# Kernel tuning notes

Measured on AMD Instinct MI355X. Metric: run time of the kernel, lower is better.

Reference implementation:

```python
import jax, jax.numpy as jnp
import numpy as np
import math

N_EMBD = 1024
N_HEAD = 16
BLOCK_SIZE = 2048
B, T = 4, 2048

def setup_inputs() -> dict:
    key = jax.random.key(0)
    ks = jax.random.split(key, 5)
    s = 0.02
    x = jax.random.normal(ks[0], (B, T, N_EMBD), dtype=jnp.float32)
    W_attn = jax.random.normal(ks[1], (N_EMBD, 3 * N_EMBD), dtype=jnp.float32) * s
    b_attn = jnp.zeros((3 * N_EMBD,), dtype=jnp.float32)
    W_proj = jax.random.normal(ks[2], (N_EMBD, N_EMBD), dtype=jnp.float32) * s
    b_proj = jnp.zeros((N_EMBD,), dtype=jnp.float32)
    return {"x": x, "W_attn": W_attn, "b_attn": b_attn, "W_proj": W_proj, "b_proj": b_proj}

def reference(x, W_attn, b_attn, W_proj, b_proj):
    b, t, c = x.shape
    hd = c // N_HEAD  # head dim
    qkv = x @ W_attn + b_attn                      # [B,T,3C]
    q, k, v = jnp.split(qkv, 3, axis=-1)
    # [B,T,C] -> [B,H,T,hd]
    q = q.reshape(b, t, N_HEAD, hd).transpose(0, 2, 1, 3)
    k = k.reshape(b, t, N_HEAD, hd).transpose(0, 2, 1, 3)
    v = v.reshape(b, t, N_HEAD, hd).transpose(0, 2, 1, 3)
    att = jnp.einsum('bhqd,bhkd->bhqk', q, k) * (1.0 / math.sqrt(hd))
    causal = jnp.tril(jnp.ones((t, t), dtype=bool))
    att = jnp.where(causal[None, None], att, -jnp.inf)
    att = jax.nn.softmax(att, axis=-1)
    y = jnp.einsum('bhqk,bhkd->bhqd', att, v)      # [B,H,T,hd]
    y = y.transpose(0, 2, 1, 3).reshape(b, t, c)
    return y @ W_proj + b_proj
```

## Files before the change

### kernel.cpp

```cpp
#include <hip/hip_runtime.h>

typedef unsigned short u16;
typedef __bf16 bf16x8 __attribute__((ext_vector_type(8)));
typedef float    f32x4 __attribute__((ext_vector_type(4)));
typedef unsigned short u16x8 __attribute__((ext_vector_type(8)));

__device__ __forceinline__ float bf2f(u16 v){ return __uint_as_float(((unsigned int)v) << 16); }
__device__ __forceinline__ u16 f2bf(float f){
    unsigned int u = __float_as_uint(f);
    u += 0x7fffu + ((u >> 16) & 1u);
    return (u16)(u >> 16);
}
__device__ __forceinline__ u16 f2bf_t(float f){ return (u16)(__float_as_uint(f) >> 16); }
__device__ __forceinline__ unsigned pack_trunc(float hi, float lo){
    return __builtin_amdgcn_perm(__float_as_uint(hi), __float_as_uint(lo), 0x07060302);
}
__device__ __forceinline__ float exp2_fast(float x){
    float r; asm("v_exp_f32 %0, %1" : "=v"(r) : "v"(x)); return r;
}

__device__ __forceinline__ void glds16(const u16* gp, u16* lp){
    __builtin_amdgcn_global_load_lds((unsigned int __attribute__((address_space(1)))*)gp,
                                     (unsigned int __attribute__((address_space(3)))*)lp,
                                     16, 0, 0);
}

__device__ __forceinline__ int probe_f32(const u16* __restrict__ xp){
    u16 lo = xp[2 * (threadIdx.x & 63)];
    int e = (lo >> 7) & 0xff;
    bool bad = !(e == 0 || (e > 96 && e < 160));
    return __popcll(__ballot(bad)) > 16;
}

__global__ __launch_bounds__(256) void conv_x(const void* __restrict__ src, u16* __restrict__ dst,
                                              const u16* __restrict__ xprobe){
    const int isf32 = probe_f32(xprobe);
    size_t i = ((size_t)blockIdx.x * 256 + threadIdx.x) * 8;
    if (isf32){
        const float* p = (const float*)src + i;
        float4 a = *(const float4*)p, b = *(const float4*)(p + 4);
        u16x8 o = { f2bf(a.x), f2bf(a.y), f2bf(a.z), f2bf(a.w),
                    f2bf(b.x), f2bf(b.y), f2bf(b.z), f2bf(b.w) };
        *(u16x8*)(dst + i) = o;
    } else {
        *(u16x8*)(dst + i) = *(const u16x8*)((const u16*)src + i);
    }
}

__global__ __launch_bounds__(256) void transposeW(const void* __restrict__ in, u16* __restrict__ out,
                                                  int R, int C, const u16* __restrict__ xprobe){
    __shared__ u16 t[64][65];
    const int isf32 = probe_f32(xprobe);
    const int c0 = blockIdx.x * 64, r0 = blockIdx.y * 64;
    const int tx = threadIdx.x & 15, ty = threadIdx.x >> 4;
#pragma unroll
    for (int i = 0; i < 4; i++){
        int r = ty + i * 16;
        u16 a, b, c, d;
        if (isf32){
            float4 v = *(const float4*)((const float*)in + (size_t)(r0 + r) * C + c0 + tx * 4);
            a = f2bf(v.x); b = f2bf(v.y); c = f2bf(v.z); d = f2bf(v.w);
        } else {
            ushort4 v = *(const ushort4*)((const u16*)in + (size_t)(r0 + r) * C + c0 + tx * 4);
            a = v.x; b = v.y; c = v.z; d = v.w;
        }
        t[r][tx*4+0] = a; t[r][tx*4+1] = b; t[r][tx*4+2] = c; t[r][tx*4+3] = d;
    }
    __syncthreads();
#pragma unroll
    for (int i = 0; i < 4; i++){
        int oc = ty + i * 16;
        ushort4 v;
        v.x = t[tx*4+0][oc]; v.y = t[tx*4+1][oc]; v.z = t[tx*4+2][oc]; v.w = t[tx*4+3][oc];
        *(ushort4*)(out + (size_t)(c0 + oc) * R + r0 + tx * 4) = v;
    }
}

#define CTS 136
template<int MODE>
__global__ __launch_bounds__(256) void gemm128(
    const u16* __restrict__ A, const u16* __restrict__ Bt, const void* __restrict__ bias,
    void* __restrict__ C, u16* __restrict__ Cq, u16* __restrict__ Ck, u16* __restrict__ Cv,
    const u16* __restrict__ xprobe, int M, int N, int K)
{
    __shared__ u16 Asm[128 * 32];
    __shared__ u16 Bsm[128 * 32];
    __shared__ u16 Ct[128 * CTS];
    const int isf32 = probe_f32(xprobe);
    const int tid = threadIdx.x;
    const int wave = tid >> 6, lane = tid & 63;
    const int quad = lane >> 4, ml = lane & 15;
    const int m_blk = blockIdx.y * 128;
    const int n_blk = blockIdx.x * 128;
    const int wm = (wave >> 1) * 64, wn = (wave & 1) * 64;
    const int rsub = lane >> 2;
    const int kc   = lane & 3;

    f32x4 acc[4][4];
#pragma unroll
    for (int a = 0; a < 4; a++)
#pragma unroll
        for (int b = 0; b < 4; b++)
            acc[a][b] = (f32x4){0.f, 0.f, 0.f, 0.f};

    for (int k0 = 0; k0 < K; k0 += 32){
        __syncthreads();
#pragma unroll
        for (int i = 0; i < 2; i++){
            int row = (wave * 2 + i) * 16 + rsub;
            glds16(A  + (size_t)(m_blk + row) * K + k0 + kc * 8, Asm + (wave * 2 + i) * 512);
            glds16(Bt + (size_t)(n_blk + row) * K + k0 + kc * 8, Bsm + (wave * 2 + i) * 512);
        }
        __syncthreads();
        bf16x8 af[4], bfr[4];
#pragma unroll
        for (int mt = 0; mt < 4; mt++) af[mt]  = *(const bf16x8*)&Asm[(wm + mt * 16 + ml) * 32 + quad * 8];
#pragma unroll
        for (int nt = 0; nt < 4; nt++) bfr[nt] = *(const bf16x8*)&Bsm[(wn + nt * 16 + ml) * 32 + quad * 8];
#pragma unroll
        for (int mt = 0; mt < 4; mt++)
#pragma unroll
            for (int nt = 0; nt < 4; nt++)
                acc[mt][nt] = __builtin_amdgcn_mfma_f32_16x16x32_bf16(af[mt], bfr[nt], acc[mt][nt], 0, 0, 0);
    }

    const float QSC = 0.18033688f;
    if (MODE == 0){
        const int which = n_blk >> 10;
        const int hbase = (n_blk >> 6) & 15;
        if (which < 2){
            const float sc = (which == 0) ? QSC : 1.0f;
#pragma unroll
            for (int nt = 0; nt < 4; nt++){
                int col = wn + nt * 16 + ml;
                float bv = isf32 ? ((const float*)bias)[n_blk + col] : bf2f(((const u16*)bias)[n_blk + col]);
#pragma unroll
                for (int mt = 0; mt < 4; mt++){
                    int row0 = wm + mt * 16 + quad * 4;
#pragma unroll
                    for (int r = 0; r < 4; r++)
                        Ct[(row0 + r) * CTS + col] = f2bf_t((acc[mt][nt][r] + bv) * sc);
                }
            }
            __syncthreads();
            u16* dst0 = (which == 0) ? Cq : Ck;
            const int b = m_blk >> 11, t0 = m_blk & 2047;
#pragma unroll
            for (int i = 0; i < 8; i++){
                int u = i * 256 + tid;
                int row = u >> 4, c8 = u & 15;
                int h = hbase + (c8 >> 3), d8 = (c8 & 7) * 8;
                u16x8 v = *(const u16x8*)&Ct[row * CTS + c8 * 8];
                *(u16x8*)&dst0[(((size_t)(b * 16 + h)) * 2048 + (t0 + row)) * 64 + d8] = v;
            }
        } else {
#pragma unroll
            for (int nt = 0; nt < 4; nt++){
                int col = wn + nt * 16 + ml;
                float bv = isf32 ? ((const float*)bias)[n_blk + col] : bf2f(((const u16*)bias)[n_blk + col]);
#pragma unroll
                for (int mt = 0; mt < 4; mt++){
                    int row0 = wm + mt * 16 + quad * 4;
                    uint2 pk;
                    pk.x = pack_trunc(acc[mt][nt][1] + bv, acc[mt][nt][0] + bv);
                    pk.y = pack_trunc(acc[mt][nt][3] + bv, acc[mt][nt][2] + bv);
                    *(uint2*)&Ct[col * CTS + row0] = pk;
                }
            }
            __syncthreads();
            const int b = m_blk >> 11, t0 = m_blk & 2047;
#pragma unroll
            for (int i = 0; i < 8; i++){
                int u = i * 256 + tid;
                int col = u >> 4, c8 = u & 15;
                int h = hbase + (col >> 6), d = col & 63;
                u16x8 v = *(const u16x8*)&Ct[col * CTS + c8 * 8];
                *(u16x8*)&Cv[(((size_t)(b * 16 + h)) * 64 + d) * 2048 + t0 + c8 * 8] = v;
            }
        }
    } else {
#pragma unroll
        for (int nt = 0; nt < 4; nt++){
            int col = n_blk + wn + nt * 16 + ml;
            float bv = isf32 ? ((const float*)bias)[col] : bf2f(((const u16*)bias)[col]);
#pragma unroll
            for (int mt = 0; mt < 4; mt++){
                float o0 = acc[mt][nt][0] + bv, o1 = acc[mt][nt][1] + bv;
                float o2 = acc[mt][nt][2] + bv, o3 = acc[mt][nt][3] + bv;
                int row0 = m_blk + wm + mt * 16 + quad * 4;
                if (isf32){
                    float* p = (float*)C + (size_t)row0 * N + col;
                    p[0] = o0; p[N] = o1; p[2*N] = o2; p[3*N] = o3;
                } else {
                    u16* p = (u16*)C + (size_t)row0 * N + col;
                    p[0] = f2bf(o0); p[N] = f2bf(o1); p[2*N] = f2bf(o2); p[3*N] = f2bf(o3);
                }
            }
        }
    }
}

#define PS 136
__global__ __launch_bounds__(256) void attn_kernel(
    const u16* __restrict__ Q, const u16* __restrict__ K, const u16* __restrict__ Vt,
    u16* __restrict__ Y)
{
    __shared__ u16 Ksm[128 * 64];
    __shared__ u16 Vsm[64 * 128];
    __shared__ u16 Psm[4][32 * PS];

    const int tid = threadIdx.x, wave = tid >> 6, lane = tid & 63;
    const int quad = lane >> 4, ml = lane & 15;
    const int flat = blockIdx.x;
    const int qb = 15 - (flat >> 6);
    const int rest = flat & 63;
    const int bh = ((rest & 7) << 3) | (rest >> 3);
    const int q0 = qb * 128;
    const size_t base = (size_t)bh * (2048 * 64);
    const float NEG = -1.0e30f;

    bf16x8 qf[2][2];
#pragma unroll
    for (int mt = 0; mt < 2; mt++)
#pragma unroll
        for (int ks = 0; ks < 2; ks++)
            qf[mt][ks] = *(const bf16x8*)(Q + base + (size_t)(q0 + mt * 64 + wave * 16 + ml) * 64 + ks * 32 + quad * 8);

    f32x4 acc[2][4];
#pragma unroll
    for (int mt = 0; mt < 2; mt++)
#pragma unroll
        for (int nt = 0; nt < 4; nt++) acc[mt][nt] = (f32x4){0.f, 0.f, 0.f, 0.f};
    float l[2][4];
#pragma unroll
    for (int mt = 0; mt < 2; mt++)
#pragma unroll
        for (int r = 0; r < 4; r++) l[mt][r] = 0.f;

    const int ntj = qb + 1;
    for (int j = 0; j < ntj; j++){
        const int j0 = j * 128;
        __syncthreads();
#pragma unroll
        for (int i = 0; i < 4; i++){
            int ub = i * 256 + wave * 64;
            int u = ub + lane;
            int row = u >> 3, cg = (lane & 7) ^ (row & 7);
            glds16(K + base + (size_t)(j0 + row) * 64 + cg * 8, Ksm + ub * 8);
            int d = u >> 4, vg = (lane & 15) ^ (d & 15);
            glds16(Vt + base + (size_t)d * 2048 + j0 + vg * 8, Vsm + ub * 8);
        }
        __syncthreads();
        const bool lastj = (j == ntj - 1);

#pragma unroll
        for (int nt = 0; nt < 8; nt++){
            bf16x8 bk0 = *(const bf16x8*)&Ksm[(nt * 16 + ml) * 64 + ((quad)     ^ (ml & 7)) * 8];
            bf16x8 bk1 = *(const bf16x8*)&Ksm[(nt * 16 + ml) * 64 + ((4 + quad) ^ (ml & 7)) * 8];
            f32x4 z = {0.f, 0.f, 0.f, 0.f};
            f32x4 s0 = __builtin_amdgcn_mfma_f32_16x16x32_bf16(qf[0][0], bk0, z, 0, 0, 0);
            s0 = __builtin_amdgcn_mfma_f32_16x16x32_bf16(qf[0][1], bk1, s0, 0, 0, 0);
            f32x4 s1 = __builtin_amdgcn_mfma_f32_16x16x32_bf16(qf[1][0], bk0, z, 0, 0, 0);
            s1 = __builtin_amdgcn_mfma_f32_16x16x32_bf16(qf[1][1], bk1, s1, 0, 0, 0);
            if (lastj){
                int cl = nt * 16 + ml;
                int r0 = wave * 16 + quad * 4;
#pragma unroll
                for (int r = 0; r < 4; r++){
                    if (cl > r0 + r)      s0[r] = NEG;
                    if (cl > 64 + r0 + r) s1[r] = NEG;
                }
            }
#pragma unroll
            for (int r = 0; r < 4; r++){
                float p0 = exp2_fast(s0[r]); l[0][r] += p0;
                Psm[wave][(quad * 4 + r) * PS + nt * 16 + ml] = f2bf_t(p0);
                float p1 = exp2_fast(s1[r]); l[1][r] += p1;
                Psm[wave][(16 + quad * 4 + r) * PS + nt * 16 + ml] = f2bf_t(p1);
            }
        }
#pragma unroll
        for (int ks = 0; ks < 4; ks++){
            bf16x8 pf0 = *(const bf16x8*)&Psm[wave][ml * PS + ks * 32 + quad * 8];
            bf16x8 pf1 = *(const bf16x8*)&Psm[wave][(16 + ml) * PS + ks * 32 + quad * 8];
#pragma unroll
            for (int nt = 0; nt < 4; nt++){
                bf16x8 vf = *(const bf16x8*)&Vsm[(nt * 16 + ml) * 128 + (((ks * 4 + quad) ^ ml) & 15) * 8];
                acc[0][nt] = __builtin_amdgcn_mfma_f32_16x16x32_bf16(pf0, vf, acc[0][nt], 0, 0, 0);
                acc[1][nt] = __builtin_amdgcn_mfma_f32_16x16x32_bf16(pf1, vf, acc[1][nt], 0, 0, 0);
            }
        }
    }
    const int b = bh >> 4, h = bh & 15;
#pragma unroll
    for (int mt = 0; mt < 2; mt++){
        f32x4 inv;
#pragma unroll
        for (int r = 0; r < 4; r++){
            float t = l[mt][r];
            t += __shfl_xor(t, 1, 64);
            t += __shfl_xor(t, 2, 64);
            t += __shfl_xor(t, 4, 64);
            t += __shfl_xor(t, 8, 64);
            inv[r] = 1.0f / t;
        }
#pragma unroll
        for (int nt = 0; nt < 4; nt++)
#pragma unroll
            for (int r = 0; r < 4; r++){
                size_t row = (size_t)b * 2048 + q0 + mt * 64 + wave * 16 + quad * 4 + r;
                Y[row * 1024 + h * 64 + nt * 16 + ml] = f2bf(acc[mt][nt][r] * inv[r]);
            }
    }
}

extern "C" void kernel_launch(void* const* d_in, const int* in_sizes, int n_in,
                              void* d_out, int out_size, void* d_ws, size_t ws_size,
                              hipStream_t stream) {
    const void* x      = d_in[0];
    const void* W_attn = d_in[1];
    const void* b_attn = d_in[2];
    const void* W_proj = d_in[3];
    const void* b_proj = d_in[4];
    const u16* xprobe = (const u16*)x;

    u16* ws = (u16*)d_ws;
    u16* Qw = ws;
    u16* Kw = ws + 8u * 1024 * 1024;
    u16* Vw = ws + 16u * 1024 * 1024;
    u16* R  = ws + 24u * 1024 * 1024;
    u16* Wt_attn = R;
    u16* Yw      = R;
    u16* Wt_proj = Qw;
    u16* xb = (u16*)d_out;

    conv_x<<<4096, 256, 0, stream>>>(x, xb, xprobe);
    transposeW<<<dim3(48, 16), 256, 0, stream>>>(W_attn, Wt_attn, 1024, 3072, xprobe);
    gemm128<0><<<dim3(24, 64), 256, 0, stream>>>(
        xb, Wt_attn, b_attn, nullptr, Qw, Kw, Vw, xprobe, 8192, 3072, 1024);
    attn_kernel<<<1024, 256, 0, stream>>>(Qw, Kw, Vw, Yw);
    transposeW<<<dim3(16, 16), 256, 0, stream>>>(W_proj, Wt_proj, 1024, 1024, xprobe);
    gemm128<1><<<dim3(8, 64), 256, 0, stream>>>(
        Yw, Wt_proj, b_proj, d_out, nullptr, nullptr, nullptr, xprobe, 8192, 1024, 1024);
}
```

Measured before the change: 263.6 us.

## Rewrite GEMM as 256x256 tiles with 4-stage async LDS pipeline

Replaces the 128x128 single-buffered GEMM with a 256x256-tile, 512-thread kernel. It uses a four-stage global_load_lds ring with explicit vmcnt waits and barriers, swizzled LDS layout to reduce bank conflicts, s_setprio around MFMA bursts, and XCD-aware block remapping. The goal is to hide global load latency and raise arithmetic intensity per tile. The trade-offs are 128KB of LDS and a larger accumulator register footprint, which limit occupancy. Grid counts also drop to 384 and 128 blocks, which may underfill the device for the projection GEMM.

Measured after the change: 266.6 us. No clear change (+1.1%).

```diff
diff --git a/kernel.cpp b/kernel.cpp
--- a/kernel.cpp
+++ b/kernel.cpp
@@ -76,118 +76,174 @@
     }
 }
 
-#define CTS 136
+#define BAR()    asm volatile("s_barrier" ::: "memory")
+#define WAITV(n) asm volatile("s_waitcnt vmcnt(" #n ")" ::: "memory")
+
 template<int MODE>
-__global__ __launch_bounds__(256) void gemm128(
+__global__ __launch_bounds__(512, 2) void gemm256(
     const u16* __restrict__ A, const u16* __restrict__ Bt, const void* __restrict__ bias,
     void* __restrict__ C, u16* __restrict__ Cq, u16* __restrict__ Ck, u16* __restrict__ Cv,
     const u16* __restrict__ xprobe, int M, int N, int K)
 {
-    __shared__ u16 Asm[128 * 32];
-    __shared__ u16 Bsm[128 * 32];
-    __shared__ u16 Ct[128 * CTS];
+    __shared__ u16 lds[65536];
     const int isf32 = probe_f32(xprobe);
     const int tid = threadIdx.x;
     const int wave = tid >> 6, lane = tid & 63;
     const int quad = lane >> 4, ml = lane & 15;
-    const int m_blk = blockIdx.y * 128;
-    const int n_blk = blockIdx.x * 128;
-    const int wm = (wave >> 1) * 64, wn = (wave & 1) * 64;
-    const int rsub = lane >> 2;
-    const int kc   = lane & 3;
-
-    f32x4 acc[4][4];
-#pragma unroll
-    for (int a = 0; a < 4; a++)
+    const int wm = wave >> 2, wn = wave & 3;
+
+    const int nbx = gridDim.x;
+    int flat = blockIdx.y * nbx + blockIdx.x;
+    const int cpx = (nbx * gridDim.y) >> 3;
+    flat = (flat & 7) * cpx + (flat >> 3);
+    const int m_blk = (flat / nbx) * 256;
+    const int n_blk = (flat % nbx) * 256;
+
+    const int rowb = tid >> 2;
+    const int swz  = (tid & 3) ^ ((tid >> 3) & 3);
+    const u16* a0 = A  + (size_t)(m_blk + rowb) * K + swz * 8;
+    const u16* a1 = a0 + (size_t)128 * K;
+    const u16* b0 = Bt + (size_t)(n_blk + rowb) * K + swz * 8;
+    const u16* b1 = b0 + (size_t)128 * K;
+    u16* ldA = lds + wave * 512;
+    u16* ldB = lds + 8192 + wave * 512;
+
+    const int fsw  = (quad ^ ((ml >> 1) & 3)) * 8;
+    const int aoff = (wm * 128 + ml) * 32 + fsw;
+    const int boff = (wn * 64  + ml) * 32 + fsw;
+
+    f32x4 acc[8][4];
+#pragma unroll
+    for (int a = 0; a < 8; a++)
 #pragma unroll
         for (int b = 0; b < 4; b++)
             acc[a][b] = (f32x4){0.f, 0.f, 0.f, 0.f};
 
-    for (int k0 = 0; k0 < K; k0 += 32){
-        __syncthreads();
-#pragma unroll
-        for (int i = 0; i < 2; i++){
-            int row = (wave * 2 + i) * 16 + rsub;
-            glds16(A  + (size_t)(m_blk + row) * K + k0 + kc * 8, Asm + (wave * 2 + i) * 512);
-            glds16(Bt + (size_t)(n_blk + row) * K + k0 + kc * 8, Bsm + (wave * 2 + i) * 512);
-        }
-        __syncthreads();
-        bf16x8 af[4], bfr[4];
-#pragma unroll
-        for (int mt = 0; mt < 4; mt++) af[mt]  = *(const bf16x8*)&Asm[(wm + mt * 16 + ml) * 32 + quad * 8];
-#pragma unroll
-        for (int nt = 0; nt < 4; nt++) bfr[nt] = *(const bf16x8*)&Bsm[(wn + nt * 16 + ml) * 32 + quad * 8];
-#pragma unroll
-        for (int mt = 0; mt < 4; mt++)
+    const int T = K >> 5;
+
+#define STAGE_A(t) { const int s_ = ((t) & 3) * 16384; const size_t ko_ = (size_t)(t) * 32; \
+    glds16(a0 + ko_, ldA + s_); glds16(a1 + ko_, ldA + s_ + 4096); }
+#define STAGE_B(t) { const int s_ = ((t) & 3) * 16384; const size_t ko_ = (size_t)(t) * 32; \
+    glds16(b0 + ko_, ldB + s_); glds16(b1 + ko_, ldB + s_ + 4096); }
+
+    STAGE_A(0); STAGE_B(0); STAGE_A(1); STAGE_B(1); STAGE_A(2); STAGE_B(2);
+    WAITV(8);
+    BAR();
+
+    for (int t = 0; t < T; ++t){
+        const u16* Ls = lds + (t & 3) * 16384;
+        bf16x8 af[4], bf[4];
+        if (t + 3 < T) STAGE_A(t + 3);
+#pragma unroll
+        for (int nt = 0; nt < 4; nt++) bf[nt] = *(const bf16x8*)&Ls[8192 + boff + nt * 512];
+#pragma unroll
+        for (int i = 0; i < 4; i++)    af[i] = *(const bf16x8*)&Ls[aoff + i * 512];
+        __builtin_amdgcn_s_setprio(1);
+#pragma unroll
+        for (int i = 0; i < 4; i++)
 #pragma unroll
             for (int nt = 0; nt < 4; nt++)
-                acc[mt][nt] = __builtin_amdgcn_mfma_f32_16x16x32_bf16(af[mt], bfr[nt], acc[mt][nt], 0, 0, 0);
-    }
+                acc[i][nt] = __builtin_amdgcn_mfma_f32_16x16x32_bf16(af[i], bf[nt], acc[i][nt], 0, 0, 0);
+        __builtin_amdgcn_s_setprio(0);
+        BAR();
+        if (t + 3 < T) STAGE_B(t + 3);
+#pragma unroll
+        for (int i = 0; i < 4; i++)    af[i] = *(const bf16x8*)&Ls[aoff + (4 + i) * 512];
+        __builtin_amdgcn_s_setprio(1);
+#pragma unroll
+        for (int i = 0; i < 4; i++)
+#pragma unroll
+            for (int nt = 0; nt < 4; nt++)
+                acc[4 + i][nt] = __builtin_amdgcn_mfma_f32_16x16x32_bf16(af[i], bf[nt], acc[4 + i][nt], 0, 0, 0);
+        __builtin_amdgcn_s_setprio(0);
+        if (t < T - 3)       { WAITV(8); }
+        else if (t == T - 3) { WAITV(4); }
+        else if (t == T - 2) { WAITV(0); }
+        BAR();
+    }
+#undef STAGE_A
+#undef STAGE_B
 
     const float QSC = 0.18033688f;
     if (MODE == 0){
+        __syncthreads();
         const int which = n_blk >> 10;
         const int hbase = (n_blk >> 6) & 15;
+        const int b = m_blk >> 11, t0 = m_blk & 2047;
         if (which < 2){
             const float sc = (which == 0) ? QSC : 1.0f;
-#pragma unroll
-            for (int nt = 0; nt < 4; nt++){
-                int col = wn + nt * 16 + ml;
-                float bv = isf32 ? ((const float*)bias)[n_blk + col] : bf2f(((const u16*)bias)[n_blk + col]);
-#pragma unroll
-                for (int mt = 0; mt < 4; mt++){
-                    int row0 = wm + mt * 16 + quad * 4;
-#pragma unroll
-                    for (int r = 0; r < 4; r++)
-                        Ct[(row0 + r) * CTS + col] = f2bf_t((acc[mt][nt][r] + bv) * sc);
-                }
-            }
-            __syncthreads();
             u16* dst0 = (which == 0) ? Cq : Ck;
-            const int b = m_blk >> 11, t0 = m_blk & 2047;
-#pragma unroll
-            for (int i = 0; i < 8; i++){
-                int u = i * 256 + tid;
-                int row = u >> 4, c8 = u & 15;
-                int h = hbase + (c8 >> 3), d8 = (c8 & 7) * 8;
-                u16x8 v = *(const u16x8*)&Ct[row * CTS + c8 * 8];
-                *(u16x8*)&dst0[(((size_t)(b * 16 + h)) * 2048 + (t0 + row)) * 64 + d8] = v;
+            u16* Ct = lds;
+#pragma unroll
+            for (int hn = 0; hn < 2; hn++){
+                if ((wn >> 1) == hn){
+#pragma unroll
+                    for (int nt = 0; nt < 4; nt++){
+                        int col = (wn & 1) * 64 + nt * 16 + ml;
+                        int gc  = n_blk + hn * 128 + col;
+                        float bv = isf32 ? ((const float*)bias)[gc] : bf2f(((const u16*)bias)[gc]);
+#pragma unroll
+                        for (int mt = 0; mt < 8; mt++){
+                            int row0 = wm * 128 + mt * 16 + quad * 4;
+#pragma unroll
+                            for (int r = 0; r < 4; r++)
+                                Ct[(row0 + r) * 136 + col] = f2bf_t((acc[mt][nt][r] + bv) * sc);
+                        }
+                    }
+                }
+                __syncthreads();
+#pragma unroll
+                for (int i = 0; i < 8; i++){
+                    int u = i * 512 + tid;
+                    int row = u >> 4, c8 = u & 15;
+                    int h = hbase + hn * 2 + (c8 >> 3), d8 = (c8 & 7) * 8;
+                    u16x8 v = *(const u16x8*)&Ct[row * 136 + c8 * 8];
+                    *(u16x8*)&dst0[(((size_t)(b * 16 + h)) * 2048 + (t0 + row)) * 64 + d8] = v;
+                }
+                __syncthreads();
             }
         } else {
-#pragma unroll
-            for (int nt = 0; nt < 4; nt++){
-                int col = wn + nt * 16 + ml;
-                float bv = isf32 ? ((const float*)bias)[n_blk + col] : bf2f(((const u16*)bias)[n_blk + col]);
-#pragma unroll
-                for (int mt = 0; mt < 4; mt++){
-                    int row0 = wm + mt * 16 + quad * 4;
-                    uint2 pk;
-                    pk.x = pack_trunc(acc[mt][nt][1] + bv, acc[mt][nt][0] + bv);
-                    pk.y = pack_trunc(acc[mt][nt][3] + bv, acc[mt][nt][2] + bv);
-                    *(uint2*)&Ct[col * CTS + row0] = pk;
-                }
-            }
-            __syncthreads();
-            const int b = m_blk >> 11, t0 = m_blk & 2047;
-#pragma unroll
-            for (int i = 0; i < 8; i++){
-                int u = i * 256 + tid;
-                int col = u >> 4, c8 = u & 15;
-                int h = hbase + (col >> 6), d = col & 63;
-                u16x8 v = *(const u16x8*)&Ct[col * CTS + c8 * 8];
-                *(u16x8*)&Cv[(((size_t)(b * 16 + h)) * 64 + d) * 2048 + t0 + c8 * 8] = v;
+            u16* Ct = lds;
+#pragma unroll
+            for (int hn = 0; hn < 2; hn++){
+                if ((wn >> 1) == hn){
+#pragma unroll
+                    for (int nt = 0; nt < 4; nt++){
+                        int col = (wn & 1) * 64 + nt * 16 + ml;
+                        int gc  = n_blk + hn * 128 + col;
+                        float bv = isf32 ? ((const float*)bias)[gc] : bf2f(((const u16*)bias)[gc]);
+#pragma unroll
+                        for (int mt = 0; mt < 8; mt++){
+                            int row0 = wm * 128 + mt * 16 + quad * 4;
+                            uint2 pk;
+                            pk.x = pack_trunc(acc[mt][nt][1] + bv, acc[mt][nt][0] + bv);
+                            pk.y = pack_trunc(acc[mt][nt][3] + bv, acc[mt][nt][2] + bv);
+                            *(uint2*)&Ct[col * 264 + row0] = pk;
+                        }
+                    }
+                }
+                __syncthreads();
+#pragma unroll
+                for (int i = 0; i < 8; i++){
+                    int u = i * 512 + tid;
+                    int col = u >> 5, c8 = u & 31;
+                    int h = hbase + hn * 2 + (col >> 6), d = col & 63;
+                    u16x8 v = *(const u16x8*)&Ct[col * 264 + c8 * 8];
+                    *(u16x8*)&Cv[(((size_t)(b * 16 + h)) * 64 + d) * 2048 + t0 + c8 * 8] = v;
+                }
+                __syncthreads();
             }
         }
     } else {
 #pragma unroll
         for (int nt = 0; nt < 4; nt++){
-            int col = n_blk + wn + nt * 16 + ml;
+            int col = n_blk + wn * 64 + nt * 16 + ml;
             float bv = isf32 ? ((const float*)bias)[col] : bf2f(((const u16*)bias)[col]);
 #pragma unroll
-            for (int mt = 0; mt < 4; mt++){
+            for (int mt = 0; mt < 8; mt++){
+                int row0 = m_blk + wm * 128 + mt * 16 + quad * 4;
                 float o0 = acc[mt][nt][0] + bv, o1 = acc[mt][nt][1] + bv;
                 float o2 = acc[mt][nt][2] + bv, o3 = acc[mt][nt][3] + bv;
-                int row0 = m_blk + wm + mt * 16 + quad * 4;
                 if (isf32){
                     float* p = (float*)C + (size_t)row0 * N + col;
                     p[0] = o0; p[N] = o1; p[2*N] = o2; p[3*N] = o3;
@@ -336,10 +392,10 @@
 
     conv_x<<<4096, 256, 0, stream>>>(x, xb, xprobe);
     transposeW<<<dim3(48, 16), 256, 0, stream>>>(W_attn, Wt_attn, 1024, 3072, xprobe);
-    gemm128<0><<<dim3(24, 64), 256, 0, stream>>>(
+    gemm256<0><<<dim3(12, 32), 512, 0, stream>>>(
         xb, Wt_attn, b_attn, nullptr, Qw, Kw, Vw, xprobe, 8192, 3072, 1024);
     attn_kernel<<<1024, 256, 0, stream>>>(Qw, Kw, Vw, Yw);
     transposeW<<<dim3(16, 16), 256, 0, stream>>>(W_proj, Wt_proj, 1024, 1024, xprobe);
-    gemm128<1><<<dim3(8, 64), 256, 0, stream>>>(
+    gemm256<1><<<dim3(4, 32), 512, 0, stream>>>(
         Yw, Wt_proj, b_proj, d_out, nullptr, nullptr, nullptr, xprobe, 8192, 1024, 1024);
 }
```

## Deepen GEMM K-tile to 64, swizzle LDS, alias epilogue buffer, remap blocks

Applied to the files above, without the earlier changes.

The bf16 GEMM kernel now stages 64-wide K slices per iteration instead of 32, which halves the number of barrier pairs per K sweep. It XOR-swizzles the 16-byte chunks in LDS to avoid bank conflicts on fragment reads. The epilogue transpose buffer now aliases the A/B staging area to keep LDS usage low, and the block index is remapped across groups of 8 so neighbouring tiles are spread, possibly for better cache or XCD locality. Risks include the extra barrier before reusing LDS and the assumption that the block count divides by 8.

After: 251.5 us. 1.05x faster.

```diff
diff --git a/kernel.cpp b/kernel.cpp
--- a/kernel.cpp
+++ b/kernel.cpp
@@ -83,18 +83,25 @@
     void* __restrict__ C, u16* __restrict__ Cq, u16* __restrict__ Ck, u16* __restrict__ Cv,
     const u16* __restrict__ xprobe, int M, int N, int K)
 {
-    __shared__ u16 Asm[128 * 32];
-    __shared__ u16 Bsm[128 * 32];
-    __shared__ u16 Ct[128 * CTS];
+    __shared__ u16 lds[17408];
+    u16* Asm = lds;
+    u16* Bsm = lds + 8192;
+    u16* Ct  = lds;
     const int isf32 = probe_f32(xprobe);
     const int tid = threadIdx.x;
     const int wave = tid >> 6, lane = tid & 63;
     const int quad = lane >> 4, ml = lane & 15;
-    const int m_blk = blockIdx.y * 128;
-    const int n_blk = blockIdx.x * 128;
+
+    const int nbx = gridDim.x;
+    int flat = blockIdx.y * nbx + blockIdx.x;
+    const int cpx = (nbx * gridDim.y) >> 3;
+    flat = (flat & 7) * cpx + (flat >> 3);
+    const int m_blk = (flat / nbx) * 128;
+    const int n_blk = (flat % nbx) * 128;
+
     const int wm = (wave >> 1) * 64, wn = (wave & 1) * 64;
-    const int rsub = lane >> 2;
-    const int kc   = lane & 3;
+    const int srow = lane >> 3;
+    const int sch  = lane & 7;
 
     f32x4 acc[4][4];
 #pragma unroll
@@ -103,26 +110,33 @@
         for (int b = 0; b < 4; b++)
             acc[a][b] = (f32x4){0.f, 0.f, 0.f, 0.f};
 
-    for (int k0 = 0; k0 < K; k0 += 32){
+    for (int k0 = 0; k0 < K; k0 += 64){
         __syncthreads();
 #pragma unroll
-        for (int i = 0; i < 2; i++){
-            int row = (wave * 2 + i) * 16 + rsub;
-            glds16(A  + (size_t)(m_blk + row) * K + k0 + kc * 8, Asm + (wave * 2 + i) * 512);
-            glds16(Bt + (size_t)(n_blk + row) * K + k0 + kc * 8, Bsm + (wave * 2 + i) * 512);
+        for (int i = 0; i < 4; i++){
+            int row = wave * 32 + i * 8 + srow;
+            int sc  = sch ^ (row & 7);
+            glds16(A  + (size_t)(m_blk + row) * K + k0 + sc * 8, Asm + (wave * 32 + i * 8) * 64);
+            glds16(Bt + (size_t)(n_blk + row) * K + k0 + sc * 8, Bsm + (wave * 32 + i * 8) * 64);
         }
         __syncthreads();
-        bf16x8 af[4], bfr[4];
-#pragma unroll
-        for (int mt = 0; mt < 4; mt++) af[mt]  = *(const bf16x8*)&Asm[(wm + mt * 16 + ml) * 32 + quad * 8];
-#pragma unroll
-        for (int nt = 0; nt < 4; nt++) bfr[nt] = *(const bf16x8*)&Bsm[(wn + nt * 16 + ml) * 32 + quad * 8];
-#pragma unroll
-        for (int mt = 0; mt < 4; mt++)
+#pragma unroll
+        for (int ks = 0; ks < 2; ks++){
+            bf16x8 af[4], bfr[4];
+#pragma unroll
+            for (int mt = 0; mt < 4; mt++)
+                af[mt]  = *(const bf16x8*)&Asm[(wm + mt * 16 + ml) * 64 + ((ks * 4 + quad) ^ (ml & 7)) * 8];
 #pragma unroll
             for (int nt = 0; nt < 4; nt++)
-                acc[mt][nt] = __builtin_amdgcn_mfma_f32_16x16x32_bf16(af[mt], bfr[nt], acc[mt][nt], 0, 0, 0);
-    }
+                bfr[nt] = *(const bf16x8*)&Bsm[(wn + nt * 16 + ml) * 64 + ((ks * 4 + quad) ^ (ml & 7)) * 8];
+#pragma unroll
+            for (int mt = 0; mt < 4; mt++)
+#pragma unroll
+                for (int nt = 0; nt < 4; nt++)
+                    acc[mt][nt] = __builtin_amdgcn_mfma_f32_16x16x32_bf16(af[mt], bfr[nt], acc[mt][nt], 0, 0, 0);
+        }
+    }
+    __syncthreads();
 
     const float QSC = 0.18033688f;
     if (MODE == 0){
```
